# Performance work log

Measured on AMD Instinct MI355X. Metric: run time of the kernel, lower is better.

The kernel has to match this reference:

```python
import jax, jax.numpy as jnp
import numpy as np

GENETIC_CODE = {'TTT': 'F', 'TTC': 'F', 'TTA': 'L', 'TTG': 'L', 'CTT': 'L', 'CTC': 'L', 'CTA': 'L', 'CTG': 'L', 'ATT': 'I', 'ATC': 'I', 'ATA': 'I', 'ATG': 'M', 'GTT': 'V', 'GTC': 'V', 'GTA': 'V', 'GTG': 'V', 'TCT': 'S', 'TCC': 'S', 'TCA': 'S', 'TCG': 'S', 'AGT': 'S', 'AGC': 'S', 'CCT': 'P', 'CCC': 'P', 'CCA': 'P', 'CCG': 'P', 'ACT': 'T', 'ACC': 'T', 'ACA': 'T', 'ACG': 'T', 'GCT': 'A', 'GCC': 'A', 'GCA': 'A', 'GCG': 'A', 'TAT': 'Y', 'TAC': 'Y', 'TAA': '*', 'TAG': '*', 'TGA': '*', 'CAT': 'H', 'CAC': 'H', 'CAA': 'Q', 'CAG': 'Q', 'AAT': 'N', 'AAC': 'N', 'AAA': 'K', 'AAG': 'K', 'GAT': 'D', 'GAC': 'D', 'GAA': 'E', 'GAG': 'E', 'TGT': 'C', 'TGC': 'C', 'TGG': 'W', 'CGT': 'R', 'CGC': 'R', 'CGA': 'R', 'CGG': 'R', 'AGA': 'R', 'AGG': 'R', 'GGT': 'G', 'GGC': 'G', 'GGA': 'G', 'GGG': 'G'}
NUC_TO_IDX = {'T': 0, 'C': 1, 'A': 2, 'G': 3}

def _build_syn_bias(synonymy_bias=1.0):
    idx = lambda c: NUC_TO_IDX[c[0]] * 16 + NUC_TO_IDX[c[1]] * 4 + NUC_TO_IDX[c[2]]
    groups = {}
    for codon, aa in GENETIC_CODE.items():
        groups.setdefault(aa, []).append(idx(codon))
    m = np.zeros((64, 64), dtype=np.float32)
    for codons in groups.values():
        for i in codons:
            for j in codons:
                m[i, j] = synonymy_bias
    return jnp.asarray(m)

HIDDEN, N_HEADS = 256, 4
HEAD_DIM = HIDDEN // N_HEADS
B, S = 2, 4096

def setup_inputs() -> dict:
    key = jax.random.key(0)
    ks = jax.random.split(key, 10)
    std = 1.0 / np.sqrt(HIDDEN)
    lin = lambda k: jax.random.uniform(k, (HIDDEN, HIDDEN), jnp.float32, -std, std)
    bias = lambda k: jax.random.uniform(k, (HIDDEN,), jnp.float32, -std, std)
    return {
        'x': jax.random.normal(ks[0], (B, S, HIDDEN), jnp.float32),
        'codons': jax.random.randint(ks[1], (B, S), 0, 64),
        'syn_bias': _build_syn_bias(1.0),
        'wq': lin(ks[2]), 'bq': bias(ks[3]),
        'wk': lin(ks[4]), 'bk': bias(ks[5]),
        'wv': lin(ks[6]), 'bv': bias(ks[7]),
        'wo': lin(ks[8]), 'bo': bias(ks[9]),
    }

def reference(x, codons, syn_bias, wq, bq, wk, bk, wv, bv, wo, bo):
    b, s, _ = x.shape
    split = lambda t: t.reshape(b, s, N_HEADS, HEAD_DIM).transpose(0, 2, 1, 3)  # (B,H,S,D)
    q = split(x @ wq.T + bq)
    k = split(x @ wk.T + bk)
    v = split(x @ wv.T + bv)
    scores = jnp.einsum('bhqd,bhkd->bhqk', q, k) / np.sqrt(HEAD_DIM)
    # gather pairwise synonymy bias: (B,S,S) broadcast over heads
    pair_bias = syn_bias[codons[:, :, None], codons[:, None, :]]
    scores = scores + pair_bias[:, None, :, :]
    attn = jax.nn.softmax(scores, axis=-1)
    out = jnp.einsum('bhqk,bhkd->bhqd', attn, v)
    out = out.transpose(0, 2, 1, 3).reshape(b, s, HIDDEN)
    return out @ wo.T + bo
```

## Files before the change

### kernel.cpp

```cpp
#include <hip/hip_runtime.h>
#include <hip/hip_bf16.h>

#define NH 4
#define HD 64
#define HID 256
#define SS 4096

#define QFRAG_PER_HEAD (128 * 6 * 64 * 8)
#define KFRAG_PER_HEAD (64 * 12 * 64 * 8)
#define VFRAG_PER_HEAD (64 * 8 * 64 * 8)

typedef float f4 __attribute__((ext_vector_type(4)));
typedef float f16v __attribute__((ext_vector_type(16)));
typedef short bf8 __attribute__((ext_vector_type(8)));
typedef unsigned int u4v __attribute__((ext_vector_type(4)));

static __device__ __forceinline__ float fast_exp2(float x) {
#if __has_builtin(__builtin_amdgcn_exp2f)
    return __builtin_amdgcn_exp2f(x);
#else
    float r; asm("v_exp_f32 %0, %1" : "=v"(r) : "v"(x)); return r;
#endif
}

static __device__ __forceinline__ unsigned pack2(float a, float b) {
    unsigned ua = (unsigned)__bfloat16_as_ushort(__float2bfloat16(a));
    unsigned ub = (unsigned)__bfloat16_as_ushort(__float2bfloat16(b));
    return ua | (ub << 16);
}

__global__ void setup_kernel(const float* __restrict__ syn,
                             int* __restrict__ gid, float* __restrict__ betaP)
{
    const int lane = threadIdx.x;
    int rep = 64;
    for (int j = 63; j >= 0; --j)
        if (syn[lane * 64 + j] != 0.0f) rep = j;
    if (rep == 64) rep = lane;
    unsigned long long m = __ballot(rep == lane);
    int id = (int)__popcll(m & ((2ull << rep) - 1ull)) - 1;
    if (id < 0) id = 0;
    gid[lane] = id;
    if (lane == 0) *betaP = syn[0] * 1.44269504088896f;
}

__global__ __launch_bounds__(256)
void pack_w_kernel(const float* __restrict__ wq, const float* __restrict__ wk,
                   const float* __restrict__ wv, const float* __restrict__ wo,
                   __hip_bfloat16* __restrict__ wpk)
{
    const int t = blockIdx.x * 256 + threadIdx.x;
    const int mat = t >> 13;
    const int r = t & 8191;
    const int dt = r >> 10, ks = (r >> 6) & 15, lane = r & 63;
    const float* w = (mat == 0) ? wq : (mat == 1) ? wk : (mat == 2) ? wv : wo;
    const int row = dt * 32 + (lane & 31);
    const int col = ks * 16 + (lane >> 5) * 8;
    const f4 a = *(const f4*)&w[(size_t)row * 256 + col];
    const f4 b = *(const f4*)&w[(size_t)row * 256 + col + 4];
    union { unsigned u[4]; bf8 v; } o;
    o.u[0] = pack2(a[0], a[1]); o.u[1] = pack2(a[2], a[3]);
    o.u[2] = pack2(b[0], b[1]); o.u[3] = pack2(b[2], b[3]);
    *(bf8*)&wpk[(size_t)t * 8] = o.v;
}

__global__ __launch_bounds__(256)
void qkv_mfma_kernel(const float* __restrict__ x,
                     const __hip_bfloat16* __restrict__ wpk,
                     const float* __restrict__ bq, const float* __restrict__ bk,
                     const float* __restrict__ bv,
                     const int* __restrict__ codons,
                     const int* __restrict__ gid, const float* __restrict__ betaP,
                     __hip_bfloat16* __restrict__ qfrag,
                     __hip_bfloat16* __restrict__ kfrag,
                     __hip_bfloat16* __restrict__ vfrag)
{
    const int bid = blockIdx.x;
    const int stile = bid / 6;
    const int grp = bid % 6;
    const int tid = threadIdx.x;
    const int w = tid >> 6, lane = tid & 63, hi = lane >> 5, l5 = lane & 31;

    const int bidx = stile >> 7;
    const int stl = stile & 127;
    const int hs = stl & 1, tkv = stl >> 1;

    __shared__ __hip_bfloat16 xs[32][256];

    {
        const int r0 = tid >> 5, c = tid & 31;
        #pragma unroll
        for (int it = 0; it < 4; ++it) {
            const int row = r0 + it * 8;
            const f4 a = *(const f4*)&x[(size_t)(stile * 32 + row) * HID + c * 8];
            const f4 b2 = *(const f4*)&x[(size_t)(stile * 32 + row) * HID + c * 8 + 4];
            union { unsigned u[4]; bf8 v; } o;
            o.u[0] = pack2(a[0], a[1]); o.u[1] = pack2(a[2], a[3]);
            o.u[2] = pack2(b2[0], b2[1]); o.u[3] = pack2(b2[2], b2[3]);
            *(bf8*)&xs[row][((c ^ row) & 31) * 8] = o.v;
        }
    }
    __syncthreads();

    const int t24 = grp * 4 + w;
    const int mat = t24 >> 3;
    const int dt = t24 & 7;
    const int head = dt >> 1, d32 = dt & 1;

    const __hip_bfloat16* wb = wpk + (size_t)((mat * 8 + dt) * 16) * 512 + (size_t)lane * 8;
    bf8 wf[16];
    #pragma unroll
    for (int ks = 0; ks < 16; ++ks) wf[ks] = *(const bf8*)&wb[ks * 512];

    f16v acc;
    #pragma unroll
    for (int r = 0; r < 16; ++r) acc[r] = 0.0f;

    if (mat < 2) {
        #pragma unroll
        for (int ks = 0; ks < 16; ++ks) {
            const bf8 xf = *(const bf8*)&xs[l5][(((ks * 2 + hi) ^ l5) & 31) * 8];
            acc = __builtin_amdgcn_mfma_f32_32x32x16_bf16(wf[ks], xf, acc, 0, 0, 0);
        }
    } else {
        #pragma unroll
        for (int ks = 0; ks < 16; ++ks) {
            const bf8 xf = *(const bf8*)&xs[l5][(((ks * 2 + hi) ^ l5) & 31) * 8];
            acc = __builtin_amdgcn_mfma_f32_32x32x16_bf16(xf, wf[ks], acc, 0, 0, 0);
        }
    }

    const float QSCALE = 0.18033688011112042f;
    if (mat == 0) {
        f4 b4[4];
        #pragma unroll
        for (int j = 0; j < 4; ++j)
            b4[j] = *(const f4*)&bq[head * 64 + d32 * 32 + j * 8 + 4 * hi];
        #pragma unroll
        for (int r = 0; r < 16; ++r) acc[r] = (acc[r] + b4[r >> 2][r & 3]) * QSCALE;
    } else if (mat == 1) {
        f4 b4[4];
        #pragma unroll
        for (int j = 0; j < 4; ++j)
            b4[j] = *(const f4*)&bk[head * 64 + d32 * 32 + j * 8 + 4 * hi];
        #pragma unroll
        for (int r = 0; r < 16; ++r) acc[r] += b4[r >> 2][r & 3];
    } else {
        const float bn = bv[head * 64 + d32 * 32 + l5];
        #pragma unroll
        for (int r = 0; r < 16; ++r) acc[r] += bn;
    }

    unsigned wd[8];
    #pragma unroll
    for (int i = 0; i < 8; ++i) wd[i] = pack2(acc[2 * i], acc[2 * i + 1]);
    const unsigned e0 = (unsigned)__shfl_xor((int)(hi ? wd[0] : wd[2]), 32, 64);
    const unsigned e1 = (unsigned)__shfl_xor((int)(hi ? wd[1] : wd[3]), 32, 64);
    const unsigned e2 = (unsigned)__shfl_xor((int)(hi ? wd[4] : wd[6]), 32, 64);
    const unsigned e3 = (unsigned)__shfl_xor((int)(hi ? wd[5] : wd[7]), 32, 64);
    union { unsigned u[4]; bf8 v; } fa, fb;
    if (hi == 0) {
        fa.u[0] = wd[0]; fa.u[1] = wd[1]; fa.u[2] = e0; fa.u[3] = e1;
        fb.u[0] = wd[4]; fb.u[1] = wd[5]; fb.u[2] = e2; fb.u[3] = e3;
    } else {
        fa.u[0] = e0; fa.u[1] = e1; fa.u[2] = wd[2]; fa.u[3] = wd[3];
        fb.u[0] = e2; fb.u[1] = e3; fb.u[2] = wd[6]; fb.u[3] = wd[7];
    }

    const int hd = bidx * NH + head;
    if (mat == 0) {
        __hip_bfloat16* qb = qfrag + (size_t)hd * QFRAG_PER_HEAD;
        *(bf8*)&qb[((size_t)(stl * 6 + d32 * 2 + 0) * 64 + lane) * 8] = fa.v;
        *(bf8*)&qb[((size_t)(stl * 6 + d32 * 2 + 1) * 64 + lane) * 8] = fb.v;
    } else if (mat == 1) {
        __hip_bfloat16* kb = kfrag + (size_t)hd * KFRAG_PER_HEAD;
        *(bf8*)&kb[((size_t)(tkv * 12 + d32 * 4 + hs) * 64 + lane) * 8] = fa.v;
        *(bf8*)&kb[((size_t)(tkv * 12 + d32 * 4 + 2 + hs) * 64 + lane) * 8] = fb.v;
    } else {
        __hip_bfloat16* vb = vfrag + (size_t)hd * VFRAG_PER_HEAD;
        const int ja = ((stl * 2 + 0) & 3) * 2 + d32;
        const int jb = ((stl * 2 + 1) & 3) * 2 + d32;
        *(bf8*)&vb[((size_t)(tkv * 8 + ja) * 64 + lane) * 8] = fa.v;
        *(bf8*)&vb[((size_t)(tkv * 8 + jb) * 64 + lane) * 8] = fb.v;
    }

    if (grp == 0) {
        const int hh = w;
        const int hd2 = bidx * NH + hh;
        __hip_bfloat16* qb = qfrag + (size_t)hd2 * QFRAG_PER_HEAD;
        __hip_bfloat16* kb = kfrag + (size_t)hd2 * KFRAG_PER_HEAD;
        u4v z; z[0] = 0; z[1] = 0; z[2] = 0; z[3] = 0;
        *(u4v*)&qb[((size_t)(stl * 6 + 4) * 64 + lane) * 8] = z;
        *(u4v*)&qb[((size_t)(stl * 6 + 5) * 64 + lane) * 8] = z;
        *(u4v*)&kb[((size_t)(tkv * 12 + 8 + hs) * 64 + lane) * 8] = z;
        *(u4v*)&kb[((size_t)(tkv * 12 + 10 + hs) * 64 + lane) * 8] = z;
        asm volatile("s_waitcnt vmcnt(0)" ::: "memory");
        if (hi == 0) {
            const int cg = gid[codons[bidx * SS + stl * 32 + l5] & 63];
            const float bl2e = *betaP;
            const int lt = ((cg >> 3) & 1) * 32 + l5;
            qb[((size_t)(stl * 6 + 4 + (cg >> 4)) * 64 + lt) * 8 + (cg & 7)] =
                __float2bfloat16(bl2e);
            kb[((size_t)(tkv * 12 + 8 + (cg >> 4) * 2 + hs) * 64 + lt) * 8 + (cg & 7)] =
                __float2bfloat16(1.0f);
        }
    }
}

__global__ __launch_bounds__(256, 2)
void attn_kernel(const __hip_bfloat16* __restrict__ qfrag,
                 const __hip_bfloat16* __restrict__ kfrag,
                 const __hip_bfloat16* __restrict__ vfrag,
                 __hip_bfloat16* __restrict__ po0,
                 __hip_bfloat16* __restrict__ po1,
                 float* __restrict__ ls0,
                 float* __restrict__ ls1)
{
    const int bid = blockIdx.x;
    const int bh = bid & 7;
    const int b = bh >> 2, h = bh & 3;
    const int idx = bid >> 3;
    const int half = idx & 1;
    const int qg = idx >> 1;
    const int tid = threadIdx.x;
    const int w = tid >> 6;
    const int lane = tid & 63;
    const int q5 = lane & 31;
    const int hi = lane >> 5;

    __shared__ __align__(16) char smem[40960];
    __shared__ float l_sh[128];

    const char* kT = (const char*)(kfrag + (size_t)(b * NH + h) * KFRAG_PER_HEAD);
    const char* vT = (const char*)(vfrag + (size_t)(b * NH + h) * VFRAG_PER_HEAD);

    const int stl = qg * 4 + w;
    const __hip_bfloat16* qb = qfrag + (size_t)(b * NH + h) * QFRAG_PER_HEAD
                               + ((size_t)stl * 6 * 64 + lane) * 8;
    bf8 qf[6];
    #pragma unroll
    for (int ks = 0; ks < 6; ++ks) qf[ks] = *(const bf8*)&qb[ks * 512];

    f16v oacc0, oacc1;
    #pragma unroll
    for (int r = 0; r < 16; ++r) { oacc0[r] = 0.0f; oacc1[r] = 0.0f; }
    float lrun = 0.0f;

    const int w5 = w * 5;
    bf8 g[5];

    auto loadG = [&](int tt) {
        #pragma unroll
        for (int c = 0; c < 5; ++c) {
            const int id = w5 + c;
            const char* src = (id < 12)
                ? kT + (size_t)tt * 12288 + (size_t)id * 1024
                : vT + (size_t)tt * 8192 + (size_t)(id - 12) * 1024;
            g[c] = *(const bf8*)(src + lane * 16);
        }
    };
    auto writeL = [&](int buf) {
        #pragma unroll
        for (int c = 0; c < 5; ++c) {
            const int id = w5 + c;
            *(bf8*)&smem[buf * 20480 + id * 1024 + lane * 16] = g[c];
        }
    };

    const int tt0 = half * 32;
    loadG(tt0);
    writeL(0);
    __syncthreads();

    int cur = 0;
    #pragma unroll 1
    for (int t = 0; t < 32; ++t) {
        if (t + 1 < 32) loadG(tt0 + t + 1);

        const char* kb = smem + cur * 20480 + lane * 16;

        f16v sA, sB;
        #pragma unroll
        for (int r = 0; r < 16; ++r) { sA[r] = 0.0f; sB[r] = 0.0f; }
        __builtin_amdgcn_s_setprio(1);
        #pragma unroll
        for (int ks = 0; ks < 6; ++ks) {
            const bf8 k0 = *(const bf8*)(kb + (2 * ks) * 1024);
            const bf8 k1 = *(const bf8*)(kb + (2 * ks + 1) * 1024);
            sA = __builtin_amdgcn_mfma_f32_32x32x16_bf16(k0, qf[ks], sA, 0, 0, 0);
            sB = __builtin_amdgcn_mfma_f32_32x32x16_bf16(k1, qf[ks], sB, 0, 0, 0);
        }
        __builtin_amdgcn_s_setprio(0);

        float ls = 0.0f;
        #pragma unroll
        for (int r = 0; r < 16; ++r) { sA[r] = fast_exp2(sA[r]); ls += sA[r]; }
        #pragma unroll
        for (int r = 0; r < 16; ++r) { sB[r] = fast_exp2(sB[r]); ls += sB[r]; }
        lrun += ls;

        unsigned dwv[2][4][2];
        #pragma unroll
        for (int j = 0; j < 4; ++j)
            #pragma unroll
            for (int c = 0; c < 2; ++c) {
                dwv[0][j][c] = pack2(sA[j * 4 + 2 * c], sA[j * 4 + 2 * c + 1]);
                dwv[1][j][c] = pack2(sB[j * 4 + 2 * c], sB[j * 4 + 2 * c + 1]);
            }
        unsigned rc[2][2][2];
        #pragma unroll
        for (int t2 = 0; t2 < 2; ++t2)
            #pragma unroll
            for (int k1 = 0; k1 < 2; ++k1)
                #pragma unroll
                for (int c = 0; c < 2; ++c) {
                    const unsigned snd = hi ? dwv[t2][2 * k1][c] : dwv[t2][2 * k1 + 1][c];
                    rc[t2][k1][c] = (unsigned)__shfl_xor((int)snd, 32, 64);
                }
        bf8 pfv[4];
        #pragma unroll
        for (int ks = 0; ks < 4; ++ks) {
            const int t2 = ks >> 1, k1 = ks & 1;
            union { unsigned u[4]; bf8 v; } pu;
            pu.u[0] = hi ? rc[t2][k1][0] : dwv[t2][2 * k1][0];
            pu.u[1] = hi ? rc[t2][k1][1] : dwv[t2][2 * k1][1];
            pu.u[2] = hi ? dwv[t2][2 * k1 + 1][0] : rc[t2][k1][0];
            pu.u[3] = hi ? dwv[t2][2 * k1 + 1][1] : rc[t2][k1][1];
            pfv[ks] = pu.v;
        }

        __builtin_amdgcn_s_setprio(1);
        #pragma unroll
        for (int ks = 0; ks < 4; ++ks) {
            const bf8 v0 = *(const bf8*)(kb + (12 + 2 * ks) * 1024);
            const bf8 v1 = *(const bf8*)(kb + (13 + 2 * ks) * 1024);
            oacc0 = __builtin_amdgcn_mfma_f32_32x32x16_bf16(v0, pfv[ks], oacc0, 0, 0, 0);
            oacc1 = __builtin_amdgcn_mfma_f32_32x32x16_bf16(v1, pfv[ks], oacc1, 0, 0, 0);
        }
        __builtin_amdgcn_s_setprio(0);

        if (t + 1 < 32) writeL(cur ^ 1);
        __syncthreads();
        cur ^= 1;
    }

    const float ltot = lrun + __shfl_xor(lrun, 32, 64);
    float* osh = (float*)smem;
    #pragma unroll
    for (int r = 0; r < 16; ++r) {
        const int d = (r & 3) + 8 * (r >> 2) + 4 * hi;
        osh[(w * 32 + q5) * 68 + d] = oacc0[r];
        osh[(w * 32 + q5) * 68 + 32 + d] = oacc1[r];
    }
    if (hi == 0) l_sh[w * 32 + q5] = ltot;
    __syncthreads();

    __hip_bfloat16* pob = half ? po1 : po0;
    float* lsb = half ? ls1 : ls0;
    const int row = tid >> 1;
    const int dh = (tid & 1) * 32;
    const float* src = &osh[row * 68 + dh];
    __hip_bfloat16* dst = pob + ((size_t)(b * SS + qg * 128 + row) * HID + h * HD + dh);
    #pragma unroll
    for (int j = 0; j < 4; ++j) {
        const f4 x0 = *(const f4*)&src[j * 8];
        const f4 x1 = *(const f4*)&src[j * 8 + 4];
        union { unsigned u[4]; bf8 v; } o;
        o.u[0] = pack2(x0[0], x0[1]); o.u[1] = pack2(x0[2], x0[3]);
        o.u[2] = pack2(x1[0], x1[1]); o.u[3] = pack2(x1[2], x1[3]);
        *(bf8*)&dst[j * 8] = o.v;
    }
    if (tid < 128) lsb[(size_t)(b * SS + qg * 128 + tid) * 4 + h] = l_sh[tid];
}

__global__ __launch_bounds__(256)
void out_proj_kernel(const __hip_bfloat16* __restrict__ po0,
                     const __hip_bfloat16* __restrict__ po1,
                     const float* __restrict__ ls0,
                     const float* __restrict__ ls1,
                     const __hip_bfloat16* __restrict__ wpk,
                     const float* __restrict__ bo, float* __restrict__ out)
{
    const int bid = blockIdx.x;
    const int stile = bid >> 1, grp = bid & 1;
    const int tid = threadIdx.x;
    const int w = tid >> 6, lane = tid & 63, hi = lane >> 5, l5 = lane & 31;

    __shared__ __hip_bfloat16 xs[32][256];
    {
        const int r0 = tid >> 5, c = tid & 31;
        #pragma unroll
        for (int it = 0; it < 4; ++it) {
            const int row = r0 + it * 8;
            const size_t srow = (size_t)stile * 32 + row;
            const int head = c >> 3;
            const float inv = 1.0f / (ls0[srow * 4 + head] + ls1[srow * 4 + head]);
            union { bf8 v; unsigned u[4]; } a0, a1;
            a0.v = *(const bf8*)&po0[srow * 256 + c * 8];
            a1.v = *(const bf8*)&po1[srow * 256 + c * 8];
            union { unsigned u[4]; bf8 v; } o;
            #pragma unroll
            for (int i = 0; i < 4; ++i) {
                const float lo = __uint_as_float(a0.u[i] << 16)
                               + __uint_as_float(a1.u[i] << 16);
                const float hv = __uint_as_float(a0.u[i] & 0xffff0000u)
                               + __uint_as_float(a1.u[i] & 0xffff0000u);
                o.u[i] = pack2(lo * inv, hv * inv);
            }
            *(bf8*)&xs[row][((c ^ row) & 31) * 8] = o.v;
        }
    }
    __syncthreads();

    const int nt = grp * 4 + w;
    const __hip_bfloat16* wb = wpk + (size_t)((3 * 8 + nt) * 16) * 512 + (size_t)lane * 8;
    bf8 wf[16];
    #pragma unroll
    for (int ks = 0; ks < 16; ++ks) wf[ks] = *(const bf8*)&wb[ks * 512];

    f16v acc;
    #pragma unroll
    for (int r = 0; r < 16; ++r) acc[r] = 0.0f;
    #pragma unroll
    for (int ks = 0; ks < 16; ++ks) {
        const bf8 xf = *(const bf8*)&xs[l5][(((ks * 2 + hi) ^ l5) & 31) * 8];
        acc = __builtin_amdgcn_mfma_f32_32x32x16_bf16(xf, wf[ks], acc, 0, 0, 0);
    }

    const float bn = bo[nt * 32 + l5];
    #pragma unroll
    for (int r = 0; r < 16; ++r) {
        const int sloc = (r & 3) + 8 * (r >> 2) + 4 * hi;
        out[(size_t)(stile * 32 + sloc) * HID + nt * 32 + l5] = acc[r] + bn;
    }
}

extern "C" void kernel_launch(void* const* d_in, const int* in_sizes, int n_in,
                              void* d_out, int out_size, void* d_ws, size_t ws_size,
                              hipStream_t stream)
{
    (void)in_sizes; (void)n_in; (void)out_size; (void)ws_size;
    const float* x        = (const float*)d_in[0];
    const int*   codons   = (const int*)d_in[1];
    const float* syn_bias = (const float*)d_in[2];
    const float* wq = (const float*)d_in[3];
    const float* bq = (const float*)d_in[4];
    const float* wk = (const float*)d_in[5];
    const float* bk = (const float*)d_in[6];
    const float* wv = (const float*)d_in[7];
    const float* bv = (const float*)d_in[8];
    const float* wo = (const float*)d_in[9];
    const float* bo = (const float*)d_in[10];
    float* out = (float*)d_out;

    char* ws = (char*)d_ws;
    int*   gid   = (int*)(ws);
    float* betaP = (float*)(ws + 256);
    __hip_bfloat16* wpk   = (__hip_bfloat16*)(ws + 4096);
    __hip_bfloat16* qfrag = (__hip_bfloat16*)(ws + (size_t)1048576u);
    __hip_bfloat16* kfrag = (__hip_bfloat16*)(ws + (size_t)7340032u);
    __hip_bfloat16* vfrag = (__hip_bfloat16*)(ws + (size_t)13631488u);
    __hip_bfloat16* po0   = (__hip_bfloat16*)(ws + (size_t)17825792u);
    __hip_bfloat16* po1   = (__hip_bfloat16*)(ws + (size_t)22020096u);
    float* ls0            = (float*)(ws + (size_t)26214400u);
    float* ls1            = (float*)(ws + (size_t)26345472u);

    setup_kernel<<<1, 64, 0, stream>>>(syn_bias, gid, betaP);
    pack_w_kernel<<<128, 256, 0, stream>>>(wq, wk, wv, wo, wpk);
    qkv_mfma_kernel<<<1536, 256, 0, stream>>>(x, wpk, bq, bk, bv, codons, gid, betaP,
                                              qfrag, kfrag, vfrag);
    attn_kernel<<<512, 256, 0, stream>>>(qfrag, kfrag, vfrag, po0, po1, ls0, ls1);
    out_proj_kernel<<<512, 256, 0, stream>>>(po0, po1, ls0, ls1, wpk, bo, out);
}
```

Measured before the change: 84.17 us.

## Process two query tiles per wave and split keys into four partitions

Each wave now holds two 32-row query tiles and reuses every K/V fragment loaded into shared memory for both. This halves LDS traffic per unit of MFMA work. To keep the same 512-block grid, the key range is split into quarters instead of halves. Four partial outputs and row sums are then merged in the out-projection kernel. The cost is higher register pressure from four accumulators and two score sets, plus extra partial-buffer traffic in both kernels.

After: 88.08 us. 1.05x slower.

```diff
diff --git a/kernel.cpp b/kernel.cpp
--- a/kernel.cpp
+++ b/kernel.cpp
@@ -213,15 +213,17 @@
                  const __hip_bfloat16* __restrict__ vfrag,
                  __hip_bfloat16* __restrict__ po0,
                  __hip_bfloat16* __restrict__ po1,
-                 float* __restrict__ ls0,
-                 float* __restrict__ ls1)
+                 __hip_bfloat16* __restrict__ po2,
+                 __hip_bfloat16* __restrict__ po3,
+                 float* __restrict__ ls0, float* __restrict__ ls1,
+                 float* __restrict__ ls2, float* __restrict__ ls3)
 {
     const int bid = blockIdx.x;
     const int bh = bid & 7;
     const int b = bh >> 2, h = bh & 3;
-    const int idx = bid >> 3;
-    const int half = idx & 1;
-    const int qg = idx >> 1;
+    const int rest = bid >> 3;
+    const int quarter = rest & 3;
+    const int qg = rest >> 2;
     const int tid = threadIdx.x;
     const int w = tid >> 6;
     const int lane = tid & 63;
@@ -234,17 +236,22 @@
     const char* kT = (const char*)(kfrag + (size_t)(b * NH + h) * KFRAG_PER_HEAD);
     const char* vT = (const char*)(vfrag + (size_t)(b * NH + h) * VFRAG_PER_HEAD);
 
-    const int stl = qg * 4 + w;
+    const int stl0 = qg * 8 + w * 2;
     const __hip_bfloat16* qb = qfrag + (size_t)(b * NH + h) * QFRAG_PER_HEAD
-                               + ((size_t)stl * 6 * 64 + lane) * 8;
-    bf8 qf[6];
-    #pragma unroll
-    for (int ks = 0; ks < 6; ++ks) qf[ks] = *(const bf8*)&qb[ks * 512];
-
-    f16v oacc0, oacc1;
-    #pragma unroll
-    for (int r = 0; r < 16; ++r) { oacc0[r] = 0.0f; oacc1[r] = 0.0f; }
-    float lrun = 0.0f;
+                               + ((size_t)stl0 * 6 * 64 + lane) * 8;
+    bf8 qf0[6], qf1[6];
+    #pragma unroll
+    for (int ks = 0; ks < 6; ++ks) {
+        qf0[ks] = *(const bf8*)&qb[ks * 512];
+        qf1[ks] = *(const bf8*)&qb[3072 + ks * 512];
+    }
+
+    f16v oacc00, oacc01, oacc10, oacc11;
+    #pragma unroll
+    for (int r = 0; r < 16; ++r) {
+        oacc00[r] = 0.0f; oacc01[r] = 0.0f; oacc10[r] = 0.0f; oacc11[r] = 0.0f;
+    }
+    float lrun0 = 0.0f, lrun1 = 0.0f;
 
     const int w5 = w * 5;
     bf8 g[5];
@@ -267,38 +274,7 @@
         }
     };
 
-    const int tt0 = half * 32;
-    loadG(tt0);
-    writeL(0);
-    __syncthreads();
-
-    int cur = 0;
-    #pragma unroll 1
-    for (int t = 0; t < 32; ++t) {
-        if (t + 1 < 32) loadG(tt0 + t + 1);
-
-        const char* kb = smem + cur * 20480 + lane * 16;
-
-        f16v sA, sB;
-        #pragma unroll
-        for (int r = 0; r < 16; ++r) { sA[r] = 0.0f; sB[r] = 0.0f; }
-        __builtin_amdgcn_s_setprio(1);
-        #pragma unroll
-        for (int ks = 0; ks < 6; ++ks) {
-            const bf8 k0 = *(const bf8*)(kb + (2 * ks) * 1024);
-            const bf8 k1 = *(const bf8*)(kb + (2 * ks + 1) * 1024);
-            sA = __builtin_amdgcn_mfma_f32_32x32x16_bf16(k0, qf[ks], sA, 0, 0, 0);
-            sB = __builtin_amdgcn_mfma_f32_32x32x16_bf16(k1, qf[ks], sB, 0, 0, 0);
-        }
-        __builtin_amdgcn_s_setprio(0);
-
-        float ls = 0.0f;
-        #pragma unroll
-        for (int r = 0; r < 16; ++r) { sA[r] = fast_exp2(sA[r]); ls += sA[r]; }
-        #pragma unroll
-        for (int r = 0; r < 16; ++r) { sB[r] = fast_exp2(sB[r]); ls += sB[r]; }
-        lrun += ls;
-
+    auto packP = [&](const f16v& sA, const f16v& sB, bf8 (&pfv)[4]) {
         unsigned dwv[2][4][2];
         #pragma unroll
         for (int j = 0; j < 4; ++j)
@@ -317,7 +293,6 @@
                     const unsigned snd = hi ? dwv[t2][2 * k1][c] : dwv[t2][2 * k1 + 1][c];
                     rc[t2][k1][c] = (unsigned)__shfl_xor((int)snd, 32, 64);
                 }
-        bf8 pfv[4];
         #pragma unroll
         for (int ks = 0; ks < 4; ++ks) {
             const int t2 = ks >> 1, k1 = ks & 1;
@@ -328,56 +303,123 @@
             pu.u[3] = hi ? dwv[t2][2 * k1 + 1][1] : rc[t2][k1][1];
             pfv[ks] = pu.v;
         }
+    };
+
+    const int tt0 = quarter * 16;
+    loadG(tt0);
+    writeL(0);
+    __syncthreads();
+
+    int cur = 0;
+    #pragma unroll 1
+    for (int t = 0; t < 16; ++t) {
+        if (t + 1 < 16) loadG(tt0 + t + 1);
+
+        const char* kb = smem + cur * 20480 + lane * 16;
+
+        f16v sA0, sB0, sA1, sB1;
+        #pragma unroll
+        for (int r = 0; r < 16; ++r) {
+            sA0[r] = 0.0f; sB0[r] = 0.0f; sA1[r] = 0.0f; sB1[r] = 0.0f;
+        }
+        __builtin_amdgcn_s_setprio(1);
+        #pragma unroll
+        for (int ks = 0; ks < 6; ++ks) {
+            const bf8 k0 = *(const bf8*)(kb + (2 * ks) * 1024);
+            const bf8 k1 = *(const bf8*)(kb + (2 * ks + 1) * 1024);
+            sA0 = __builtin_amdgcn_mfma_f32_32x32x16_bf16(k0, qf0[ks], sA0, 0, 0, 0);
+            sB0 = __builtin_amdgcn_mfma_f32_32x32x16_bf16(k1, qf0[ks], sB0, 0, 0, 0);
+            sA1 = __builtin_amdgcn_mfma_f32_32x32x16_bf16(k0, qf1[ks], sA1, 0, 0, 0);
+            sB1 = __builtin_amdgcn_mfma_f32_32x32x16_bf16(k1, qf1[ks], sB1, 0, 0, 0);
+        }
+        __builtin_amdgcn_s_setprio(0);
+
+        float ls = 0.0f;
+        #pragma unroll
+        for (int r = 0; r < 16; ++r) { sA0[r] = fast_exp2(sA0[r]); ls += sA0[r]; }
+        #pragma unroll
+        for (int r = 0; r < 16; ++r) { sB0[r] = fast_exp2(sB0[r]); ls += sB0[r]; }
+        lrun0 += ls;
+        bf8 pfv0[4];
+        packP(sA0, sB0, pfv0);
+
+        ls = 0.0f;
+        #pragma unroll
+        for (int r = 0; r < 16; ++r) { sA1[r] = fast_exp2(sA1[r]); ls += sA1[r]; }
+        #pragma unroll
+        for (int r = 0; r < 16; ++r) { sB1[r] = fast_exp2(sB1[r]); ls += sB1[r]; }
+        lrun1 += ls;
+        bf8 pfv1[4];
+        packP(sA1, sB1, pfv1);
 
         __builtin_amdgcn_s_setprio(1);
         #pragma unroll
         for (int ks = 0; ks < 4; ++ks) {
             const bf8 v0 = *(const bf8*)(kb + (12 + 2 * ks) * 1024);
             const bf8 v1 = *(const bf8*)(kb + (13 + 2 * ks) * 1024);
-            oacc0 = __builtin_amdgcn_mfma_f32_32x32x16_bf16(v0, pfv[ks], oacc0, 0, 0, 0);
-            oacc1 = __builtin_amdgcn_mfma_f32_32x32x16_bf16(v1, pfv[ks], oacc1, 0, 0, 0);
+            oacc00 = __builtin_amdgcn_mfma_f32_32x32x16_bf16(v0, pfv0[ks], oacc00, 0, 0, 0);
+            oacc01 = __builtin_amdgcn_mfma_f32_32x32x16_bf16(v1, pfv0[ks], oacc01, 0, 0, 0);
+            oacc10 = __builtin_amdgcn_mfma_f32_32x32x16_bf16(v0, pfv1[ks], oacc10, 0, 0, 0);
+            oacc11 = __builtin_amdgcn_mfma_f32_32x32x16_bf16(v1, pfv1[ks], oacc11, 0, 0, 0);
         }
         __builtin_amdgcn_s_setprio(0);
 
-        if (t + 1 < 32) writeL(cur ^ 1);
+        if (t + 1 < 16) writeL(cur ^ 1);
         __syncthreads();
         cur ^= 1;
     }
 
-    const float ltot = lrun + __shfl_xor(lrun, 32, 64);
+    const float ltot0 = lrun0 + __shfl_xor(lrun0, 32, 64);
+    const float ltot1 = lrun1 + __shfl_xor(lrun1, 32, 64);
+    __hip_bfloat16* pob = (quarter == 0) ? po0 : (quarter == 1) ? po1
+                        : (quarter == 2) ? po2 : po3;
+    float* lsb = (quarter == 0) ? ls0 : (quarter == 1) ? ls1
+               : (quarter == 2) ? ls2 : ls3;
     float* osh = (float*)smem;
-    #pragma unroll
-    for (int r = 0; r < 16; ++r) {
-        const int d = (r & 3) + 8 * (r >> 2) + 4 * hi;
-        osh[(w * 32 + q5) * 68 + d] = oacc0[r];
-        osh[(w * 32 + q5) * 68 + 32 + d] = oacc1[r];
-    }
-    if (hi == 0) l_sh[w * 32 + q5] = ltot;
-    __syncthreads();
-
-    __hip_bfloat16* pob = half ? po1 : po0;
-    float* lsb = half ? ls1 : ls0;
-    const int row = tid >> 1;
-    const int dh = (tid & 1) * 32;
-    const float* src = &osh[row * 68 + dh];
-    __hip_bfloat16* dst = pob + ((size_t)(b * SS + qg * 128 + row) * HID + h * HD + dh);
-    #pragma unroll
-    for (int j = 0; j < 4; ++j) {
-        const f4 x0 = *(const f4*)&src[j * 8];
-        const f4 x1 = *(const f4*)&src[j * 8 + 4];
-        union { unsigned u[4]; bf8 v; } o;
-        o.u[0] = pack2(x0[0], x0[1]); o.u[1] = pack2(x0[2], x0[3]);
-        o.u[2] = pack2(x1[0], x1[1]); o.u[3] = pack2(x1[2], x1[3]);
-        *(bf8*)&dst[j * 8] = o.v;
-    }
-    if (tid < 128) lsb[(size_t)(b * SS + qg * 128 + tid) * 4 + h] = l_sh[tid];
+
+    #pragma unroll
+    for (int pass = 0; pass < 2; ++pass) {
+        const f16v oa = pass ? oacc10 : oacc00;
+        const f16v ob = pass ? oacc11 : oacc01;
+        const float lt = pass ? ltot1 : ltot0;
+        #pragma unroll
+        for (int r = 0; r < 16; ++r) {
+            const int d = (r & 3) + 8 * (r >> 2) + 4 * hi;
+            osh[(w * 32 + q5) * 68 + d] = oa[r];
+            osh[(w * 32 + q5) * 68 + 32 + d] = ob[r];
+        }
+        if (hi == 0) l_sh[w * 32 + q5] = lt;
+        __syncthreads();
+
+        const int row = tid >> 1;
+        const int dh = (tid & 1) * 32;
+        const int brow = qg * 256 + (row >> 5) * 64 + pass * 32 + (row & 31);
+        const float* src = &osh[row * 68 + dh];
+        __hip_bfloat16* dst = pob + ((size_t)(b * SS + brow) * HID + h * HD + dh);
+        #pragma unroll
+        for (int j = 0; j < 4; ++j) {
+            const f4 x0 = *(const f4*)&src[j * 8];
+            const f4 x1 = *(const f4*)&src[j * 8 + 4];
+            union { unsigned u[4]; bf8 v; } o;
+            o.u[0] = pack2(x0[0], x0[1]); o.u[1] = pack2(x0[2], x0[3]);
+            o.u[2] = pack2(x1[0], x1[1]); o.u[3] = pack2(x1[2], x1[3]);
+            *(bf8*)&dst[j * 8] = o.v;
+        }
+        if (tid < 128) {
+            const int tr = qg * 256 + (tid >> 5) * 64 + pass * 32 + (tid & 31);
+            lsb[(size_t)(b * SS + tr) * 4 + h] = l_sh[tid];
+        }
+        __syncthreads();
+    }
 }
 
 __global__ __launch_bounds__(256)
 void out_proj_kernel(const __hip_bfloat16* __restrict__ po0,
                      const __hip_bfloat16* __restrict__ po1,
-                     const float* __restrict__ ls0,
-                     const float* __restrict__ ls1,
+                     const __hip_bfloat16* __restrict__ po2,
+                     const __hip_bfloat16* __restrict__ po3,
+                     const float* __restrict__ ls0, const float* __restrict__ ls1,
+                     const float* __restrict__ ls2, const float* __restrict__ ls3,
                      const __hip_bfloat16* __restrict__ wpk,
                      const float* __restrict__ bo, float* __restrict__ out)
 {
@@ -394,17 +436,24 @@
             const int row = r0 + it * 8;
             const size_t srow = (size_t)stile * 32 + row;
             const int head = c >> 3;
-            const float inv = 1.0f / (ls0[srow * 4 + head] + ls1[srow * 4 + head]);
-            union { bf8 v; unsigned u[4]; } a0, a1;
+            const float inv = 1.0f / (ls0[srow * 4 + head] + ls1[srow * 4 + head]
+                                    + ls2[srow * 4 + head] + ls3[srow * 4 + head]);
+            union { bf8 v; unsigned u[4]; } a0, a1, a2, a3;
             a0.v = *(const bf8*)&po0[srow * 256 + c * 8];
             a1.v = *(const bf8*)&po1[srow * 256 + c * 8];
+            a2.v = *(const bf8*)&po2[srow * 256 + c * 8];
+            a3.v = *(const bf8*)&po3[srow * 256 + c * 8];
             union { unsigned u[4]; bf8 v; } o;
             #pragma unroll
             for (int i = 0; i < 4; ++i) {
                 const float lo = __uint_as_float(a0.u[i] << 16)
-                               + __uint_as_float(a1.u[i] << 16);
+                               + __uint_as_float(a1.u[i] << 16)
+                               + __uint_as_float(a2.u[i] << 16)
+                               + __uint_as_float(a3.u[i] << 16);
                 const float hv = __uint_as_float(a0.u[i] & 0xffff0000u)
-                               + __uint_as_float(a1.u[i] & 0xffff0000u);
+                               + __uint_as_float(a1.u[i] & 0xffff0000u)
+                               + __uint_as_float(a2.u[i] & 0xffff0000u)
+                               + __uint_as_float(a3.u[i] & 0xffff0000u);
                 o.u[i] = pack2(lo * inv, hv * inv);
             }
             *(bf8*)&xs[row][((c ^ row) & 31) * 8] = o.v;
@@ -462,13 +511,19 @@
     __hip_bfloat16* vfrag = (__hip_bfloat16*)(ws + (size_t)13631488u);
     __hip_bfloat16* po0   = (__hip_bfloat16*)(ws + (size_t)17825792u);
     __hip_bfloat16* po1   = (__hip_bfloat16*)(ws + (size_t)22020096u);
-    float* ls0            = (float*)(ws + (size_t)26214400u);
-    float* ls1            = (float*)(ws + (size_t)26345472u);
+    __hip_bfloat16* po2   = (__hip_bfloat16*)(ws + (size_t)26214400u);
+    __hip_bfloat16* po3   = (__hip_bfloat16*)(ws + (size_t)30408704u);
+    float* ls0            = (float*)(ws + (size_t)34603008u);
+    float* ls1            = (float*)(ws + (size_t)34734080u);
+    float* ls2            = (float*)(ws + (size_t)34865152u);
+    float* ls3            = (float*)(ws + (size_t)34996224u);
 
     setup_kernel<<<1, 64, 0, stream>>>(syn_bias, gid, betaP);
     pack_w_kernel<<<128, 256, 0, stream>>>(wq, wk, wv, wo, wpk);
     qkv_mfma_kernel<<<1536, 256, 0, stream>>>(x, wpk, bq, bk, bv, codons, gid, betaP,
                                               qfrag, kfrag, vfrag);
-    attn_kernel<<<512, 256, 0, stream>>>(qfrag, kfrag, vfrag, po0, po1, ls0, ls1);
-    out_proj_kernel<<<512, 256, 0, stream>>>(po0, po1, ls0, ls1, wpk, bo, out);
-}
+    attn_kernel<<<512, 256, 0, stream>>>(qfrag, kfrag, vfrag,
+                                         po0, po1, po2, po3, ls0, ls1, ls2, ls3);
+    out_proj_kernel<<<512, 256, 0, stream>>>(po0, po1, po2, po3,
+                                             ls0, ls1, ls2, ls3, wpk, bo, out);
+}
```

## Software-pipeline QK^T one tile ahead with triple-buffered LDS and packed bf16 convert

Applied to the files above, without the earlier changes.

Restructures the attention main loop so the QK^T MFMAs for the next KV tile are issued before the exp/pack/PV work on the current tile, letting matrix and vector ALU work overlap. To support this, LDS grows from two to three 20 KB buffers and global loads are issued two tiles ahead. The bf16 packing also moves to the single v_cvt_pk_bf16_f32 instruction. The larger LDS footprint and the extra live score accumulators raise register pressure and may reduce occupancy.

Result: no change. 85.69 us (+1.8%).

```diff
diff --git a/kernel.cpp b/kernel.cpp
--- a/kernel.cpp
+++ b/kernel.cpp
@@ -27,6 +27,12 @@
     unsigned ua = (unsigned)__bfloat16_as_ushort(__float2bfloat16(a));
     unsigned ub = (unsigned)__bfloat16_as_ushort(__float2bfloat16(b));
     return ua | (ub << 16);
+}
+
+static __device__ __forceinline__ unsigned cvtpk(float a, float b) {
+    unsigned r;
+    asm("v_cvt_pk_bf16_f32 %0, %1, %2" : "=v"(r) : "v"(a), "v"(b));
+    return r;
 }
 
 __global__ void setup_kernel(const float* __restrict__ syn,
@@ -228,7 +234,7 @@
     const int q5 = lane & 31;
     const int hi = lane >> 5;
 
-    __shared__ __align__(16) char smem[40960];
+    __shared__ __align__(16) char smem[61440];
     __shared__ float l_sh[128];
 
     const char* kT = (const char*)(kfrag + (size_t)(b * NH + h) * KFRAG_PER_HEAD);
@@ -248,8 +254,10 @@
 
     const int w5 = w * 5;
     bf8 g[5];
-
-    auto loadG = [&](int tt) {
+    const int tt0 = half * 32;
+
+    auto loadG = [&](int t) {
+        const int tt = tt0 + t;
         #pragma unroll
         for (int c = 0; c < 5; ++c) {
             const int id = w5 + c;
@@ -266,20 +274,8 @@
             *(bf8*)&smem[buf * 20480 + id * 1024 + lane * 16] = g[c];
         }
     };
-
-    const int tt0 = half * 32;
-    loadG(tt0);
-    writeL(0);
-    __syncthreads();
-
-    int cur = 0;
-    #pragma unroll 1
-    for (int t = 0; t < 32; ++t) {
-        if (t + 1 < 32) loadG(tt0 + t + 1);
-
-        const char* kb = smem + cur * 20480 + lane * 16;
-
-        f16v sA, sB;
+    auto qk = [&](int buf, f16v& sA, f16v& sB) {
+        const char* kb = smem + buf * 20480 + lane * 16;
         #pragma unroll
         for (int r = 0; r < 16; ++r) { sA[r] = 0.0f; sB[r] = 0.0f; }
         __builtin_amdgcn_s_setprio(1);
@@ -291,12 +287,18 @@
             sB = __builtin_amdgcn_mfma_f32_32x32x16_bf16(k1, qf[ks], sB, 0, 0, 0);
         }
         __builtin_amdgcn_s_setprio(0);
+    };
+
+    int bT = 0, bT1 = 1, bT2 = 2;
+
+    auto body = [&](int t, f16v& sAc, f16v& sBc, f16v& sAn, f16v& sBn) {
+        if (t + 1 < 32) qk(bT1, sAn, sBn);
 
         float ls = 0.0f;
         #pragma unroll
-        for (int r = 0; r < 16; ++r) { sA[r] = fast_exp2(sA[r]); ls += sA[r]; }
-        #pragma unroll
-        for (int r = 0; r < 16; ++r) { sB[r] = fast_exp2(sB[r]); ls += sB[r]; }
+        for (int r = 0; r < 16; ++r) { sAc[r] = fast_exp2(sAc[r]); ls += sAc[r]; }
+        #pragma unroll
+        for (int r = 0; r < 16; ++r) { sBc[r] = fast_exp2(sBc[r]); ls += sBc[r]; }
         lrun += ls;
 
         unsigned dwv[2][4][2];
@@ -304,8 +306,8 @@
         for (int j = 0; j < 4; ++j)
             #pragma unroll
             for (int c = 0; c < 2; ++c) {
-                dwv[0][j][c] = pack2(sA[j * 4 + 2 * c], sA[j * 4 + 2 * c + 1]);
-                dwv[1][j][c] = pack2(sB[j * 4 + 2 * c], sB[j * 4 + 2 * c + 1]);
+                dwv[0][j][c] = cvtpk(sAc[j * 4 + 2 * c], sAc[j * 4 + 2 * c + 1]);
+                dwv[1][j][c] = cvtpk(sBc[j * 4 + 2 * c], sBc[j * 4 + 2 * c + 1]);
             }
         unsigned rc[2][2][2];
         #pragma unroll
@@ -329,19 +331,35 @@
             pfv[ks] = pu.v;
         }
 
+        const char* vb = smem + bT * 20480 + lane * 16;
         __builtin_amdgcn_s_setprio(1);
         #pragma unroll
         for (int ks = 0; ks < 4; ++ks) {
-            const bf8 v0 = *(const bf8*)(kb + (12 + 2 * ks) * 1024);
-            const bf8 v1 = *(const bf8*)(kb + (13 + 2 * ks) * 1024);
+            const bf8 v0 = *(const bf8*)(vb + (12 + 2 * ks) * 1024);
+            const bf8 v1 = *(const bf8*)(vb + (13 + 2 * ks) * 1024);
             oacc0 = __builtin_amdgcn_mfma_f32_32x32x16_bf16(v0, pfv[ks], oacc0, 0, 0, 0);
             oacc1 = __builtin_amdgcn_mfma_f32_32x32x16_bf16(v1, pfv[ks], oacc1, 0, 0, 0);
         }
         __builtin_amdgcn_s_setprio(0);
 
-        if (t + 1 < 32) writeL(cur ^ 1);
+        if (t + 2 < 32) writeL(bT2);
+        if (t + 3 < 32) loadG(t + 3);
         __syncthreads();
-        cur ^= 1;
+        const int tmp = bT; bT = bT1; bT1 = bT2; bT2 = tmp;
+    };
+
+    loadG(0); writeL(0); loadG(1);
+    __syncthreads();
+    f16v sA, sB, sA2, sB2;
+    qk(0, sA, sB);
+    writeL(1);
+    loadG(2);
+    __syncthreads();
+
+    #pragma unroll 1
+    for (int t = 0; t < 32; t += 2) {
+        body(t, sA, sB, sA2, sB2);
+        body(t + 1, sA2, sB2, sA, sB);
     }
 
     const float ltot = lrun + __shfl_xor(lrun, 32, 64);
```
